# Optimization experiments

Hardware: AMD Instinct MI355X
Metric: run time of the kernel (lower is better)

Reference implementation:

```python
import jax, jax.numpy as jnp
import numpy as np

PI = 3.141592653589793
TAU = 0.5          # gumbel-softmax temperature
EPS = 1e-6
B, N, D = 128, 32, 256

def _linear(x, w, b=None):
    y = x @ w.T
    return y if b is None else y + b

def _wrap(a):
    return (a + PI) % (2 * PI) - PI

def setup_inputs() -> dict:
    key = jax.random.key(0)
    ks = jax.random.split(key, 16)
    s = 0.05
    return {
        "embedding": jax.random.normal(ks[0], (B, N, 11), jnp.float32),
        "gumbel_u": jax.random.uniform(ks[1], (B * N, N - 1, 2), jnp.float32),
        "emb1_w": jax.random.normal(ks[2], (128, 5), jnp.float32) * s,
        "emb1_b": jnp.zeros((128,), jnp.float32),
        "emb2_w": jax.random.normal(ks[3], (D, 128), jnp.float32) * s,
        "emb2_b": jnp.zeros((D,), jnp.float32),
        "hm1_w": jax.random.normal(ks[4], (D, D + 7), jnp.float32) * s,
        "hm1_b": jnp.zeros((D,), jnp.float32),
        "hm2_w": jax.random.normal(ks[5], (D, D), jnp.float32) * s,
        "hm2_b": jnp.zeros((D,), jnp.float32),
        "he_w": jax.random.normal(ks[6], (2, D), jnp.float32) * s,
        "he_b": jnp.zeros((2,), jnp.float32),
        "q_w": jax.random.normal(ks[7], (D, D), jnp.float32) * s,
        "k_w": jax.random.normal(ks[8], (D, 10), jnp.float32) * s,
        "v_w": jax.random.normal(ks[9], (D, 10), jnp.float32) * s,
        "v_b": jnp.zeros((D,), jnp.float32),
        "dec_w": jax.random.normal(ks[10], (2 * D, 2 * D), jnp.float32) * s,
        "dec_b": jnp.zeros((2 * D,), jnp.float32),
    }

def reference(embedding, gumbel_u, emb1_w, emb1_b, emb2_w, emb2_b,
              hm1_w, hm1_b, hm2_w, hm2_b, he_w, he_b,
              q_w, k_w, v_w, v_b, dec_w, dec_b):
    b, n, _ = embedding.shape
    d = q_w.shape[0]
    # static off-diagonal index lists (i,j), j != i, row-major like mask indexing
    rows, cols = np.nonzero(~np.eye(n, dtype=bool))

    embed = embedding[:, :, 4:9].reshape(b * n, 5)
    position = embedding[:, :, :2]
    heading = embedding[:, :, 2:4]
    action = embedding[:, :, 7:9]
    goal = embedding[:, :, -2:]

    # agent embedding MLP (leaky_relu slope 0.01, torch default)
    h = jax.nn.leaky_relu(_linear(embed, emb1_w, emb1_b))
    agent_embed = jax.nn.leaky_relu(_linear(h, emb2_w, emb2_b)).reshape(b, n, d)

    # pairwise geometry  [b,i,j,...]
    rel_vec = position[:, None, :, :] - position[:, :, None, :]   # pos_j - pos_i
    dx, dy = rel_vec[..., 0], rel_vec[..., 1]
    rel_dist = jnp.linalg.norm(rel_vec, axis=-1, keepdims=True) / 12.0
    heading_angle_i = jnp.arctan2(heading[..., 1], heading[..., 0])[:, :, None]  # [b,n,1]
    angle = _wrap(jnp.arctan2(dy, dx) - heading_angle_i)
    hj_cos = jnp.broadcast_to(heading[:, None, :, 0], (b, n, n))
    hj_sin = jnp.broadcast_to(heading[:, None, :, 1], (b, n, n))
    action_j = jnp.broadcast_to(action[:, None, :, :], (b, n, n, 2))
    edge_features = jnp.concatenate([
        rel_dist, jnp.cos(angle)[..., None], jnp.sin(angle)[..., None],
        hj_cos[..., None], hj_sin[..., None], action_j], axis=-1)  # [b,n,n,7]

    # hard attention branch (off-diagonal pairs only)
    h_i_flat = jnp.broadcast_to(agent_embed[:, :, None, :], (b, n, n - 1, d)).reshape(b * n, n - 1, d)
    edge_flat = edge_features[:, rows, cols].reshape(b * n, n - 1, 7)
    hard_input = jnp.concatenate([h_i_flat, edge_flat], axis=-1)
    h_hard = _linear(jax.nn.relu(_linear(hard_input, hm1_w, hm1_b)), hm2_w, hm2_b)
    hard_logits = _linear(h_hard, he_w, he_b)                      # [b*n, n-1, 2]
    g = -jnp.log(-jnp.log(gumbel_u + 1e-10) + 1e-10)
    hard_soft = jax.nn.softmax((hard_logits + g) / TAU, axis=-1)
    hard_weights = hard_soft[..., 1].reshape(b, n, n - 1)

    unnorm = jnp.linalg.norm(rel_vec, axis=-1, keepdims=True)      # [b,n,n,1]
    unnorm_rel_dist = unnorm[:, rows, cols].reshape(b * n, n - 1, 1)

    # goal polar features
    goal_rel_vec = goal[:, None, :, :] - position[:, :, None, :]   # [b,n,n,2]
    goal_rel_dist = jnp.linalg.norm(goal_rel_vec, axis=-1, keepdims=True)
    goal_rel_angle = _wrap(jnp.arctan2(goal_rel_vec[..., 1], goal_rel_vec[..., 0]) - heading_angle_i)
    goal_polar = jnp.concatenate([goal_rel_dist, jnp.cos(goal_rel_angle)[..., None],
                                  jnp.sin(goal_rel_angle)[..., None]], axis=-1)
    soft_edge = jnp.concatenate([edge_features, goal_polar], axis=-1)  # [b,n,n,10]

    # soft attention (vectorized over agents; off-diagonal gather)
    q = agent_embed @ q_w.T                                         # [b,n,d]
    k = soft_edge @ k_w.T                                           # [b,n,n,d]
    v = jax.nn.relu(_linear(soft_edge, v_w, v_b))                   # [b,n,n,d]
    k_off = k[:, rows, cols].reshape(b, n, n - 1, d)
    v_off = v[:, rows, cols].reshape(b, n, n - 1, d)
    score = jnp.einsum('bnd,bnjd->bnj', q, k_off) / jnp.sqrt(jnp.float32(d))
    soft_w = jax.nn.softmax(score, axis=-1)
    combined = soft_w * hard_weights                                # [b,n,n-1]
    x = jnp.einsum('bnjd,bnj->bnd', v_off, combined).reshape(b * n, d)

    final_input = jnp.concatenate([agent_embed.reshape(b * n, d), x], axis=-1)
    output = _linear(final_input, dec_w, dec_b)                     # [b*n, 2d]

    cwn = combined / (combined.sum(axis=-1, keepdims=True) + EPS)
    mean_entropy = (-(cwn * jnp.log(cwn + EPS)).sum(axis=-1)).mean()
    comb_w = combined.reshape(n, -1)  # matches torch.stack(dim=1).reshape(n, -1)

    return (output, hard_logits[..., 1], unnorm_rel_dist, mean_entropy, hard_weights, comb_w)
```

## Files before the change

kernel.cpp:

```cpp
#include <hip/hip_runtime.h>
#include <hip/hip_bf16.h>
#include <math.h>

typedef __hip_bfloat16 bf16;
typedef short bf16x8 __attribute__((ext_vector_type(8)));
typedef float f32x4 __attribute__((ext_vector_type(4)));
typedef unsigned short u16;

#define R_TOT 4096
#define NJ 31

#define OFF_AE   0
#define OFF_QK   1048576
#define OFF_S1   2097152
#define OFF_ENT  4542464
#define OFF_X    4546560
#define OFF_W    5595136
#define W_E1W   0
#define W_E1B   640
#define W_E2P   768
#define W_E2B   33536
#define W_H1B   101120
#define W_W1EP  167684
#define W_HE2P  171780
#define W_CB    173828
#define W_S1P   200452
#define W_VW    235780
#define W_VB    238340
#define W_DECWT 238596
#define W_DECB  500740
#define W_QKM   501252

#define OUT0 0
#define OUT1 2097152
#define OUT2 2224128
#define OUT3 2351104
#define OUT4 2351105
#define OUT5 2478081

__device__ __forceinline__ float b2f(bf16 x) { return __bfloat162float(x); }
__device__ __forceinline__ float ldin(const void* p, int i, int flag) {
    return flag ? b2f(((const bf16*)p)[i]) : ((const float*)p)[i];
}
__device__ __forceinline__ void stout(void* p, int i, float v, int flag) {
    if (flag) ((bf16*)p)[i] = __float2bfloat16(v);
    else      ((float*)p)[i] = v;
}
__device__ __forceinline__ u16 f2bbits(float v) {
    bf16 h = __float2bfloat16(v);
    return *(u16*)&h;
}
__device__ __forceinline__ int detect_flag(const void* emb) {
    float x = ((const float*)emb)[threadIdx.x & 63];
    int sane = (x == x) && (fabsf(x) < 1e20f);
    unsigned long long m = __ballot(sane);
    return (__popcll(m) == 64) ? 0 : 1;
}

__global__ __launch_bounds__(256) void k_prep(
        const void* emb,
        const void* e1w, const void* e1b, const void* e2w, const void* e2b,
        const void* h1w, const void* h1b, const void* h2w, const void* h2b,
        const void* hew, const void* heb, const void* qw,  const void* kw,
        const void* vw,  const void* vb,  const void* decw,const void* decb,
        float* W) {
    int flag = detect_flag(emb);
    int blk = blockIdx.x;
    int tid = threadIdx.x;
    if (blk < 2048) {
        int idx = blk * 256 + tid;
        if (idx < 262144) {
            int jj   = idx & 7;
            int lane = (idx >> 3) & 63;
            int tile = idx >> 9;
            int nt = tile & 31, kt = tile >> 5;
            int n = nt * 16 + (lane & 15);
            int k = kt * 32 + ((lane >> 4) << 3) + jj;
            ((u16*)(W + W_DECWT))[idx] = f2bbits(ldin(decw, n * 512 + k, flag));
        }
        int j = idx - 262144;
        if (j >= 0 && j < 98304) {
            int p;
            const void* src; int ldm, Wdst;
            if (j < 32768)      { p = j;          src = e2w; ldm = 128; Wdst = W_E2P; }
            else                { p = j - 32768;  src = h1w; ldm = 263; Wdst = W_S1P; }
            int jj   = p & 7;
            int lane = (p >> 3) & 63;
            int tile = p >> 9;
            int nt = tile & 15, kt = tile >> 4;
            int n = nt * 16 + (lane & 15);
            int k = kt * 32 + ((lane >> 4) << 3) + jj;
            ((u16*)(W + Wdst))[p] = f2bbits(ldin(src, n * ldm + k, flag));
        } else if (j >= 98304 && j < 102912) {
            int q2 = j - 98304;
            if      (q2 < 640)   W[W_E1W  + q2]           = ldin(e1w,  q2,          flag);
            else if (q2 < 768)   W[W_E1B  + (q2 - 640)]   = ldin(e1b,  q2 - 640,    flag);
            else if (q2 < 1024)  W[W_E2B  + (q2 - 768)]   = ldin(e2b,  q2 - 768,    flag);
            else if (q2 < 1280)  W[W_H1B  + (q2 - 1024)]  = ldin(h1b,  q2 - 1024,   flag);
            else if (q2 < 3840)  W[W_VW   + (q2 - 1280)]  = ldin(vw,   q2 - 1280,   flag);
            else if (q2 < 4096)  W[W_VB   + (q2 - 3840)]  = ldin(vb,   q2 - 3840,   flag);
            else                 W[W_DECB + (q2 - 4096)]  = ldin(decb, q2 - 4096,   flag);
        }
    } else if (blk < 2304) {
        int p = (blk - 2048) * 16 + (tid >> 4);
        int l = tid & 15;
        int jj = p & 7, lane = (p >> 3) & 63, kt = p >> 9;
        int k = kt * 32 + ((lane >> 4) << 3) + jj;
        int n = lane & 15;
        float v = 0.f;
        if (n < 10) {
#pragma unroll
            for (int dd = 0; dd < 16; dd++) {
                int d = l + 16 * dd;
                v += ldin(qw, d * 256 + k, flag) * ldin(kw, d * 10 + n, flag);
            }
        }
        v += __shfl_xor(v, 1, 64); v += __shfl_xor(v, 2, 64);
        v += __shfl_xor(v, 4, 64); v += __shfl_xor(v, 8, 64);
        if (l == 0) ((u16*)(W + W_QKM))[p] = f2bbits(v);
    } else if (blk < 2560) {
        int q = (blk - 2304) * 16 + (tid >> 4);
        int l = tid & 15;
        int jj = q & 7, lane = (q >> 3) & 63, kt = q >> 9;
        int n = lane & 15;
        int c = kt * 32 + ((lane >> 4) << 3) + jj;
        float v = 0.f;
        if (n < 2) {
#pragma unroll
            for (int dd = 0; dd < 16; dd++) {
                int d = l + 16 * dd;
                v += ldin(hew, n * 256 + d, flag) * ldin(h2w, d * 256 + c, flag);
            }
        }
        v += __shfl_xor(v, 1, 64); v += __shfl_xor(v, 2, 64);
        v += __shfl_xor(v, 4, 64); v += __shfl_xor(v, 8, 64);
        if (l == 0) ((u16*)(W + W_HE2P))[q] = f2bbits(v);
    } else if (blk < 2592) {
        int p = (blk - 2560) * 256 + tid;
        int jj = p & 7, lane = (p >> 3) & 63, nt = p >> 9;
        int n = nt * 16 + (lane & 15);
        int k = ((lane >> 4) << 3) + jj;
        float v = (k < 7) ? ldin(h1w, n * 263 + 256 + k, flag) : 0.f;
        ((u16*)(W + W_W1EP))[p] = f2bbits(v);
    } else {
        if (tid < 32) {
            int i = tid >> 4, l = tid & 15;
            float v = 0.f;
#pragma unroll
            for (int dd = 0; dd < 16; dd++) {
                int d = l + 16 * dd;
                v += ldin(hew, i * 256 + d, flag) * ldin(h2b, d, flag);
            }
            v += __shfl_xor(v, 1, 64); v += __shfl_xor(v, 2, 64);
            v += __shfl_xor(v, 4, 64); v += __shfl_xor(v, 8, 64);
            if (l == 0) W[W_CB + i] = v + ldin(heb, i, flag);
        }
    }
}

__global__ __launch_bounds__(256) void k_embed(const void* emb, const float* W,
                                               u16* aeb, float* qkws, float* s1ws) {
    int flag = detect_flag(emb);
    int r0 = blockIdx.x * 16;
    __shared__ float embL[16][12];
    __shared__ u16 hB[16][136];
    __shared__ u16 aeB[16][264];
    int tid = threadIdx.x;
    for (int idx = tid; idx < 16 * 11; idx += 256) {
        int s = idx / 11, t = idx % 11;
        embL[s][t] = ldin(emb, (r0 + s) * 11 + t, flag);
    }
    __syncthreads();
    for (int idx = tid; idx < 16 * 128; idx += 256) {
        int s = idx >> 7, jo = idx & 127;
        float v = W[W_E1B + jo];
#pragma unroll
        for (int t = 0; t < 5; t++) v += W[W_E1W + jo * 5 + t] * embL[s][4 + t];
        hB[s][jo] = f2bbits(v > 0.f ? v : 0.01f * v);
    }
    __syncthreads();
    int wv = tid >> 6, ln = tid & 63;
    int lr = ln & 15, quad = ln >> 4;
    {
        const bf16x8* Bp = (const bf16x8*)(W + W_E2P);
        f32x4 acc[4];
#pragma unroll
        for (int nt = 0; nt < 4; nt++) acc[nt] = (f32x4){0.f, 0.f, 0.f, 0.f};
#pragma unroll
        for (int kt = 0; kt < 4; kt++) {
            bf16x8 af = *(const bf16x8*)&hB[lr][kt * 32 + (quad << 3)];
#pragma unroll
            for (int nt = 0; nt < 4; nt++) {
                bf16x8 bfr = Bp[(kt * 16 + (wv * 4 + nt)) * 64 + ln];
                acc[nt] = __builtin_amdgcn_mfma_f32_16x16x32_bf16(af, bfr, acc[nt], 0, 0, 0);
            }
        }
#pragma unroll
        for (int nt = 0; nt < 4; nt++) {
            int d = wv * 64 + nt * 16 + lr;
            float bias = W[W_E2B + d];
#pragma unroll
            for (int reg = 0; reg < 4; reg++) {
                int m = quad * 4 + reg;
                float v = acc[nt][reg] + bias;
                v = v > 0.f ? v : 0.01f * v;
                u16 bits = f2bbits(v);
                aeB[m][d] = bits;
                aeb[(r0 + m) * 256 + d] = bits;
            }
        }
    }
    __syncthreads();
    {
        const bf16x8* Bs = (const bf16x8*)(W + W_S1P);
        f32x4 sac[4];
#pragma unroll
        for (int nt = 0; nt < 4; nt++) sac[nt] = (f32x4){0.f, 0.f, 0.f, 0.f};
#pragma unroll
        for (int kt = 0; kt < 8; kt++) {
            bf16x8 af = *(const bf16x8*)&aeB[lr][kt * 32 + (quad << 3)];
#pragma unroll
            for (int nt = 0; nt < 4; nt++) {
                bf16x8 bs = Bs[(kt * 16 + (wv * 4 + nt)) * 64 + ln];
                sac[nt] = __builtin_amdgcn_mfma_f32_16x16x32_bf16(af, bs, sac[nt], 0, 0, 0);
            }
        }
#pragma unroll
        for (int nt = 0; nt < 4; nt++) {
            int d = wv * 64 + nt * 16 + lr;
            float bias = W[W_H1B + d];
#pragma unroll
            for (int reg = 0; reg < 4; reg++) {
                int m = quad * 4 + reg;
                s1ws[(r0 + m) * 256 + d] = sac[nt][reg] + bias;
            }
        }
        if (wv == 0) {
            const bf16x8* Bm = (const bf16x8*)(W + W_QKM);
            f32x4 qk = (f32x4){0.f, 0.f, 0.f, 0.f};
#pragma unroll
            for (int kt = 0; kt < 8; kt++) {
                bf16x8 af = *(const bf16x8*)&aeB[lr][kt * 32 + (quad << 3)];
                qk = __builtin_amdgcn_mfma_f32_16x16x32_bf16(af, Bm[kt * 64 + ln], qk, 0, 0, 0);
            }
            if (lr < 10) {
#pragma unroll
                for (int reg = 0; reg < 4; reg++) {
                    int m = quad * 4 + reg;
                    qkws[(r0 + m) * 10 + lr] = qk[reg];
                }
            }
        }
    }
}

__global__ __launch_bounds__(256) void k_fused(const void* emb, const void* gum,
                                               const float* s1ws, const float* qkws, const float* W,
                                               u16* xb, float* entws, void* out) {
    int flag = detect_flag(emb);
    int r = blockIdx.x;
    int b = r >> 5, i = r & 31;
    __shared__ float embB[32][12];
    __shared__ float seL[32][10];
    __shared__ u16 eA[32][32];
    __shared__ u16 a1[32][264];
    __shared__ float pj[4][32][2];
    __shared__ float cL[32];
    __shared__ float qkL[10];
    int tid = threadIdx.x;
    for (int idx = tid; idx < 32 * 11; idx += 256) {
        int s = idx / 11, t = idx % 11;
        embB[s][t] = ldin(emb, (b * 32 + s) * 11 + t, flag);
    }
    for (int idx = tid; idx < 32 * 32; idx += 256) ((u16*)eA)[idx] = 0;
    if (tid >= 64 && tid < 74) qkL[tid - 64] = qkws[r * 10 + (tid - 64)];
    __syncthreads();
    if (tid < NJ) {
        int jp = tid;
        int j = jp + (jp >= i ? 1 : 0);
        float pix = embB[i][0], piy = embB[i][1], hix = embB[i][2], hiy = embB[i][3];
        float pjx = embB[j][0], pjy = embB[j][1], hjx = embB[j][2], hjy = embB[j][3];
        float ajx = embB[j][7], ajy = embB[j][8];
        float gjx = embB[j][9], gjy = embB[j][10];
        float dx = pjx - pix, dy = pjy - piy;
        float dist = sqrtf(dx * dx + dy * dy);
        float hai = atan2f(hiy, hix);
        float ang = atan2f(dy, dx) - hai;
        float gx = gjx - pix, gy = gjy - piy;
        float gdist = sqrtf(gx * gx + gy * gy);
        float gang = atan2f(gy, gx) - hai;
        float f[10];
        f[0] = dist * (1.f / 12.f);
        f[1] = cosf(ang); f[2] = sinf(ang);
        f[3] = hjx; f[4] = hjy; f[5] = ajx; f[6] = ajy;
        f[7] = gdist; f[8] = cosf(gang); f[9] = sinf(gang);
#pragma unroll
        for (int t = 0; t < 10; t++) seL[jp][t] = f[t];
#pragma unroll
        for (int t = 0; t < 7; t++) eA[jp][t] = f2bbits(f[t]);
        stout(out, OUT2 + r * NJ + jp, dist, flag);
    }
    __syncthreads();
    int wv = tid >> 6, ln = tid & 63;
    int lr = ln & 15, quad = ln >> 4;
    {
        const bf16x8* Bp = (const bf16x8*)(W + W_W1EP);
        bf16x8 af0 = *(const bf16x8*)&eA[lr][quad << 3];
        bf16x8 af1 = *(const bf16x8*)&eA[16 + lr][quad << 3];
#pragma unroll
        for (int nt = 0; nt < 4; nt++) {
            int gnt = wv * 4 + nt;
            int d = gnt * 16 + lr;
            float s1v = s1ws[r * 256 + d];
            f32x4 acc0 = (f32x4){s1v, s1v, s1v, s1v};
            f32x4 acc1 = acc0;
            bf16x8 bb = Bp[gnt * 64 + ln];
            acc0 = __builtin_amdgcn_mfma_f32_16x16x32_bf16(af0, bb, acc0, 0, 0, 0);
            acc1 = __builtin_amdgcn_mfma_f32_16x16x32_bf16(af1, bb, acc1, 0, 0, 0);
#pragma unroll
            for (int reg = 0; reg < 4; reg++) {
                a1[(quad << 2) + reg][d]      = f2bbits(fmaxf(acc0[reg], 0.f));
                a1[16 + (quad << 2) + reg][d] = f2bbits(fmaxf(acc1[reg], 0.f));
            }
        }
    }
    __syncthreads();
    {
        const bf16x8* Ep = (const bf16x8*)(W + W_HE2P);
        f32x4 l0 = (f32x4){0.f, 0.f, 0.f, 0.f};
        f32x4 l1 = (f32x4){0.f, 0.f, 0.f, 0.f};
#pragma unroll
        for (int kk = 0; kk < 2; kk++) {
            int kt = wv * 2 + kk;
            bf16x8 a0 = *(const bf16x8*)&a1[lr][kt * 32 + (quad << 3)];
            bf16x8 a1f = *(const bf16x8*)&a1[16 + lr][kt * 32 + (quad << 3)];
            bf16x8 bb = Ep[kt * 64 + ln];
            l0 = __builtin_amdgcn_mfma_f32_16x16x32_bf16(a0, bb, l0, 0, 0, 0);
            l1 = __builtin_amdgcn_mfma_f32_16x16x32_bf16(a1f, bb, l1, 0, 0, 0);
        }
        if (lr < 2) {
#pragma unroll
            for (int reg = 0; reg < 4; reg++) {
                pj[wv][(quad << 2) + reg][lr]      = l0[reg];
                pj[wv][16 + (quad << 2) + reg][lr] = l1[reg];
            }
        }
    }
    __syncthreads();
    if (wv == 0) {
        float hwv = 0.f;
        if (ln < NJ) {
            float p0 = pj[0][ln][0] + pj[1][ln][0] + pj[2][ln][0] + pj[3][ln][0];
            float p1 = pj[0][ln][1] + pj[1][ln][1] + pj[2][ln][1] + pj[3][ln][1];
            float l0 = p0 + W[W_CB + 0], l1 = p1 + W[W_CB + 1];
            float u0 = ldin(gum, (r * NJ + ln) * 2 + 0, flag);
            float u1 = ldin(gum, (r * NJ + ln) * 2 + 1, flag);
            float g0 = -logf(-logf(u0 + 1e-10f) + 1e-10f);
            float g1 = -logf(-logf(u1 + 1e-10f) + 1e-10f);
            float dl = ((l1 + g1) - (l0 + g0)) * 2.0f;
            hwv = 1.f / (1.f + expf(-dl));
            stout(out, OUT1 + r * NJ + ln, l1, flag);
            stout(out, OUT4 + r * NJ + ln, hwv, flag);
        }
        float sc = -1e30f;
        if (ln < NJ) {
            float p = 0.f;
#pragma unroll
            for (int t = 0; t < 10; t++) p += qkL[t] * seL[ln][t];
            sc = p * (1.f / 16.f);
        }
        float m = sc;
#pragma unroll
        for (int s = 32; s >= 1; s >>= 1) m = fmaxf(m, __shfl_xor(m, s, 64));
        float e = (ln < NJ) ? expf(sc - m) : 0.f;
        float sum = e;
#pragma unroll
        for (int s = 32; s >= 1; s >>= 1) sum += __shfl_xor(sum, s, 64);
        float sw = e / sum;
        float cmb = sw * hwv;
        if (ln < NJ) {
            cL[ln] = cmb;
            stout(out, OUT5 + r * NJ + ln, cmb, flag);
        }
        float csum = cmb;
#pragma unroll
        for (int s = 32; s >= 1; s >>= 1) csum += __shfl_xor(csum, s, 64);
        float cwn = cmb / (csum + 1e-6f);
        float et = (ln < NJ) ? -cwn * logf(cwn + 1e-6f) : 0.f;
#pragma unroll
        for (int s = 32; s >= 1; s >>= 1) et += __shfl_xor(et, s, 64);
        if (ln == 0) entws[r] = et;
    }
    __syncthreads();
    float vwr[10];
#pragma unroll
    for (int t = 0; t < 10; t++) vwr[t] = W[W_VW + tid * 10 + t];
    float vbv = W[W_VB + tid];
    float x = 0.f;
    for (int j = 0; j < NJ; j++) {
        float v = vbv;
#pragma unroll
        for (int t = 0; t < 10; t++) v += vwr[t] * seL[j][t];
        v = fmaxf(v, 0.f);
        x += v * cL[j];
    }
    xb[r * 256 + tid] = f2bbits(x);
}

__global__ __launch_bounds__(256) void k_dec(const void* emb, const u16* aeb, const u16* xb,
                                             const float* W, const float* entws, void* out) {
    int flag = detect_flag(emb);
    int r0 = (blockIdx.x >> 2) * 32;
    int nq = blockIdx.x & 3;
    __shared__ u16 finB[32][520];
    int tid = threadIdx.x;
    for (int idx = tid; idx < 32 * 512; idx += 256) {
        int s = idx >> 9, c = idx & 511;
        finB[s][c] = (c < 256) ? aeb[(r0 + s) * 256 + c] : xb[(r0 + s) * 256 + (c - 256)];
    }
    __syncthreads();
    int wv = tid >> 6, ln = tid & 63;
    int lr = ln & 15, quad = ln >> 4;
    const bf16x8* Bp = (const bf16x8*)(W + W_DECWT);
    f32x4 acc[2][2];
#pragma unroll
    for (int mt = 0; mt < 2; mt++)
#pragma unroll
        for (int nt = 0; nt < 2; nt++) acc[mt][nt] = (f32x4){0.f, 0.f, 0.f, 0.f};
#pragma unroll
    for (int kt = 0; kt < 16; kt++) {
        bf16x8 af[2];
#pragma unroll
        for (int mt = 0; mt < 2; mt++)
            af[mt] = *(const bf16x8*)&finB[mt * 16 + lr][kt * 32 + (quad << 3)];
#pragma unroll
        for (int nt = 0; nt < 2; nt++) {
            int gnt = nq * 8 + wv * 2 + nt;
            bf16x8 bfr = Bp[(kt * 32 + gnt) * 64 + ln];
#pragma unroll
            for (int mt = 0; mt < 2; mt++)
                acc[mt][nt] = __builtin_amdgcn_mfma_f32_16x16x32_bf16(af[mt], bfr, acc[mt][nt], 0, 0, 0);
        }
    }
#pragma unroll
    for (int nt = 0; nt < 2; nt++) {
        int d = (nq * 8 + wv * 2 + nt) * 16 + lr;
        float bias = W[W_DECB + d];
#pragma unroll
        for (int mt = 0; mt < 2; mt++)
#pragma unroll
            for (int reg = 0; reg < 4; reg++) {
                int m = mt * 16 + quad * 4 + reg;
                stout(out, OUT0 + (r0 + m) * 512 + d, acc[mt][nt][reg] + bias, flag);
            }
    }
    if (blockIdx.x == 0) {
        __shared__ float red[4];
        float s = 0.f;
        for (int i2 = tid; i2 < R_TOT; i2 += 256) s += entws[i2];
#pragma unroll
        for (int m = 32; m >= 1; m >>= 1) s += __shfl_xor(s, m, 64);
        if ((tid & 63) == 0) red[tid >> 6] = s;
        __syncthreads();
        if (tid == 0) {
            float t = red[0] + red[1] + red[2] + red[3];
            stout(out, OUT3, t / (float)R_TOT, flag);
        }
    }
}

extern "C" void kernel_launch(void* const* d_in, const int* in_sizes, int n_in,
                              void* d_out, int out_size, void* d_ws, size_t ws_size,
                              hipStream_t stream) {
    const void* emb  = d_in[0];
    const void* gum  = d_in[1];
    const void* e1w  = d_in[2];
    const void* e1b  = d_in[3];
    const void* e2w  = d_in[4];
    const void* e2b  = d_in[5];
    const void* h1w  = d_in[6];
    const void* h1b  = d_in[7];
    const void* h2w  = d_in[8];
    const void* h2b  = d_in[9];
    const void* hew  = d_in[10];
    const void* heb  = d_in[11];
    const void* qw   = d_in[12];
    const void* kw   = d_in[13];
    const void* vw   = d_in[14];
    const void* vb   = d_in[15];
    const void* decw = d_in[16];
    const void* decb = d_in[17];

    float* wsf = (float*)d_ws;
    u16*   aeb  = (u16*)(wsf + OFF_AE);
    float* qkws = wsf + OFF_QK;
    float* s1ws = wsf + OFF_S1;
    float* entw = wsf + OFF_ENT;
    u16*   xb   = (u16*)(wsf + OFF_X);
    float* W    = wsf + OFF_W;

    hipLaunchKernelGGL(k_prep, dim3(2593), dim3(256), 0, stream,
                       emb, e1w, e1b, e2w, e2b, h1w, h1b, h2w, h2b, hew, heb,
                       qw, kw, vw, vb, decw, decb, W);
    hipLaunchKernelGGL(k_embed, dim3(256), dim3(256), 0, stream, emb, W, aeb, qkws, s1ws);
    hipLaunchKernelGGL(k_fused, dim3(4096), dim3(256), 0, stream,
                       emb, gum, s1ws, qkws, W, xb, entw, d_out);
    hipLaunchKernelGGL(k_dec, dim3(512), dim3(256), 0, stream, emb, aeb, xb, W, entw, d_out);
}
```

Before: 161.1 us.

## Move weight packing not needed by embed into the embed kernel launch

Weight-prep work is split across two kernels. The first keeps only what k_embed depends on: the e2/h1 packing, the QK product and the small vectors. The decoder weight transpose, the he·h2 product, the W1E packing and the constant bias now run as extra blocks of k_embed, so they overlap with the embedding computation. This shrinks the serial prep kernel on the critical path, at the cost of a larger k_embed grid with mixed block roles.

```diff
diff --git a/kernel.cpp b/kernel.cpp
--- a/kernel.cpp
+++ b/kernel.cpp
@@ -60,16 +60,63 @@
 __global__ __launch_bounds__(256) void k_prep(
         const void* emb,
         const void* e1w, const void* e1b, const void* e2w, const void* e2b,
-        const void* h1w, const void* h1b, const void* h2w, const void* h2b,
-        const void* hew, const void* heb, const void* qw,  const void* kw,
-        const void* vw,  const void* vb,  const void* decw,const void* decb,
+        const void* h1w, const void* h1b, const void* qw,  const void* kw,
+        const void* vw,  const void* vb,  const void* decb,
         float* W) {
     int flag = detect_flag(emb);
     int blk = blockIdx.x;
     int tid = threadIdx.x;
-    if (blk < 2048) {
-        int idx = blk * 256 + tid;
-        if (idx < 262144) {
+    if (blk < 384) {
+        int p; const void* src; int ldm, Wdst;
+        if (blk < 128) { p = blk * 256 + tid;         src = e2w; ldm = 128; Wdst = W_E2P; }
+        else           { p = (blk - 128) * 256 + tid; src = h1w; ldm = 263; Wdst = W_S1P; }
+        int jj   = p & 7;
+        int lane = (p >> 3) & 63;
+        int tile = p >> 9;
+        int nt = tile & 15, kt = tile >> 4;
+        int n = nt * 16 + (lane & 15);
+        int k = kt * 32 + ((lane >> 4) << 3) + jj;
+        ((u16*)(W + Wdst))[p] = f2bbits(ldin(src, n * ldm + k, flag));
+    } else if (blk < 640) {
+        int p = (blk - 384) * 16 + (tid >> 4);
+        int l = tid & 15;
+        int jj = p & 7, lane = (p >> 3) & 63, kt = p >> 9;
+        int k = kt * 32 + ((lane >> 4) << 3) + jj;
+        int n = lane & 15;
+        float v = 0.f;
+        if (n < 10) {
+#pragma unroll
+            for (int dd = 0; dd < 16; dd++) {
+                int d = l + 16 * dd;
+                v += ldin(qw, d * 256 + k, flag) * ldin(kw, d * 10 + n, flag);
+            }
+        }
+        v += __shfl_xor(v, 1, 64); v += __shfl_xor(v, 2, 64);
+        v += __shfl_xor(v, 4, 64); v += __shfl_xor(v, 8, 64);
+        if (l == 0) ((u16*)(W + W_QKM))[p] = f2bbits(v);
+    } else {
+        int q2 = (blk - 640) * 256 + tid;
+        if      (q2 < 640)   W[W_E1W  + q2]           = ldin(e1w,  q2,          flag);
+        else if (q2 < 768)   W[W_E1B  + (q2 - 640)]   = ldin(e1b,  q2 - 640,    flag);
+        else if (q2 < 1024)  W[W_E2B  + (q2 - 768)]   = ldin(e2b,  q2 - 768,    flag);
+        else if (q2 < 1280)  W[W_H1B  + (q2 - 1024)]  = ldin(h1b,  q2 - 1024,   flag);
+        else if (q2 < 3840)  W[W_VW   + (q2 - 1280)]  = ldin(vw,   q2 - 1280,   flag);
+        else if (q2 < 4096)  W[W_VB   + (q2 - 3840)]  = ldin(vb,   q2 - 3840,   flag);
+        else if (q2 < 4608)  W[W_DECB + (q2 - 4096)]  = ldin(decb, q2 - 4096,   flag);
+    }
+}
+
+__global__ __launch_bounds__(256) void k_embed(const void* emb, const float* W_,
+                                               const void* h1w, const void* h2w, const void* h2b,
+                                               const void* hew, const void* heb, const void* decw,
+                                               u16* aeb, float* qkws, float* s1ws) {
+    int flag = detect_flag(emb);
+    float* W = (float*)W_;
+    int blk = blockIdx.x;
+    int tid = threadIdx.x;
+    if (blk >= 256) {
+        if (blk < 1280) {
+            int idx = (blk - 256) * 256 + tid;
             int jj   = idx & 7;
             int lane = (idx >> 3) & 63;
             int tile = idx >> 9;
@@ -77,95 +124,50 @@
             int n = nt * 16 + (lane & 15);
             int k = kt * 32 + ((lane >> 4) << 3) + jj;
             ((u16*)(W + W_DECWT))[idx] = f2bbits(ldin(decw, n * 512 + k, flag));
-        }
-        int j = idx - 262144;
-        if (j >= 0 && j < 98304) {
-            int p;
-            const void* src; int ldm, Wdst;
-            if (j < 32768)      { p = j;          src = e2w; ldm = 128; Wdst = W_E2P; }
-            else                { p = j - 32768;  src = h1w; ldm = 263; Wdst = W_S1P; }
-            int jj   = p & 7;
-            int lane = (p >> 3) & 63;
-            int tile = p >> 9;
-            int nt = tile & 15, kt = tile >> 4;
+        } else if (blk < 1312) {
+            int p = (blk - 1280) * 256 + tid;
+            int jj = p & 7, lane = (p >> 3) & 63, nt = p >> 9;
             int n = nt * 16 + (lane & 15);
-            int k = kt * 32 + ((lane >> 4) << 3) + jj;
-            ((u16*)(W + Wdst))[p] = f2bbits(ldin(src, n * ldm + k, flag));
-        } else if (j >= 98304 && j < 102912) {
-            int q2 = j - 98304;
-            if      (q2 < 640)   W[W_E1W  + q2]           = ldin(e1w,  q2,          flag);
-            else if (q2 < 768)   W[W_E1B  + (q2 - 640)]   = ldin(e1b,  q2 - 640,    flag);
-            else if (q2 < 1024)  W[W_E2B  + (q2 - 768)]   = ldin(e2b,  q2 - 768,    flag);
-            else if (q2 < 1280)  W[W_H1B  + (q2 - 1024)]  = ldin(h1b,  q2 - 1024,   flag);
-            else if (q2 < 3840)  W[W_VW   + (q2 - 1280)]  = ldin(vw,   q2 - 1280,   flag);
-            else if (q2 < 4096)  W[W_VB   + (q2 - 3840)]  = ldin(vb,   q2 - 3840,   flag);
-            else                 W[W_DECB + (q2 - 4096)]  = ldin(decb, q2 - 4096,   flag);
-        }
-    } else if (blk < 2304) {
-        int p = (blk - 2048) * 16 + (tid >> 4);
-        int l = tid & 15;
-        int jj = p & 7, lane = (p >> 3) & 63, kt = p >> 9;
-        int k = kt * 32 + ((lane >> 4) << 3) + jj;
-        int n = lane & 15;
-        float v = 0.f;
-        if (n < 10) {
-#pragma unroll
-            for (int dd = 0; dd < 16; dd++) {
-                int d = l + 16 * dd;
-                v += ldin(qw, d * 256 + k, flag) * ldin(kw, d * 10 + n, flag);
-            }
-        }
-        v += __shfl_xor(v, 1, 64); v += __shfl_xor(v, 2, 64);
-        v += __shfl_xor(v, 4, 64); v += __shfl_xor(v, 8, 64);
-        if (l == 0) ((u16*)(W + W_QKM))[p] = f2bbits(v);
-    } else if (blk < 2560) {
-        int q = (blk - 2304) * 16 + (tid >> 4);
-        int l = tid & 15;
-        int jj = q & 7, lane = (q >> 3) & 63, kt = q >> 9;
-        int n = lane & 15;
-        int c = kt * 32 + ((lane >> 4) << 3) + jj;
-        float v = 0.f;
-        if (n < 2) {
-#pragma unroll
-            for (int dd = 0; dd < 16; dd++) {
-                int d = l + 16 * dd;
-                v += ldin(hew, n * 256 + d, flag) * ldin(h2w, d * 256 + c, flag);
-            }
-        }
-        v += __shfl_xor(v, 1, 64); v += __shfl_xor(v, 2, 64);
-        v += __shfl_xor(v, 4, 64); v += __shfl_xor(v, 8, 64);
-        if (l == 0) ((u16*)(W + W_HE2P))[q] = f2bbits(v);
-    } else if (blk < 2592) {
-        int p = (blk - 2560) * 256 + tid;
-        int jj = p & 7, lane = (p >> 3) & 63, nt = p >> 9;
-        int n = nt * 16 + (lane & 15);
-        int k = ((lane >> 4) << 3) + jj;
-        float v = (k < 7) ? ldin(h1w, n * 263 + 256 + k, flag) : 0.f;
-        ((u16*)(W + W_W1EP))[p] = f2bbits(v);
-    } else {
-        if (tid < 32) {
-            int i = tid >> 4, l = tid & 15;
+            int k = ((lane >> 4) << 3) + jj;
+            float v = (k < 7) ? ldin(h1w, n * 263 + 256 + k, flag) : 0.f;
+            ((u16*)(W + W_W1EP))[p] = f2bbits(v);
+        } else if (blk < 1568) {
+            int q = (blk - 1312) * 16 + (tid >> 4);
+            int l = tid & 15;
+            int jj = q & 7, lane = (q >> 3) & 63, kt = q >> 9;
+            int n = lane & 15;
+            int c = kt * 32 + ((lane >> 4) << 3) + jj;
             float v = 0.f;
-#pragma unroll
-            for (int dd = 0; dd < 16; dd++) {
-                int d = l + 16 * dd;
-                v += ldin(hew, i * 256 + d, flag) * ldin(h2b, d, flag);
+            if (n < 2) {
+#pragma unroll
+                for (int dd = 0; dd < 16; dd++) {
+                    int d = l + 16 * dd;
+                    v += ldin(hew, n * 256 + d, flag) * ldin(h2w, d * 256 + c, flag);
+                }
             }
             v += __shfl_xor(v, 1, 64); v += __shfl_xor(v, 2, 64);
             v += __shfl_xor(v, 4, 64); v += __shfl_xor(v, 8, 64);
-            if (l == 0) W[W_CB + i] = v + ldin(heb, i, flag);
-        }
-    }
-}
-
-__global__ __launch_bounds__(256) void k_embed(const void* emb, const float* W,
-                                               u16* aeb, float* qkws, float* s1ws) {
-    int flag = detect_flag(emb);
-    int r0 = blockIdx.x * 16;
+            if (l == 0) ((u16*)(W + W_HE2P))[q] = f2bbits(v);
+        } else {
+            if (tid < 32) {
+                int i = tid >> 4, l = tid & 15;
+                float v = 0.f;
+#pragma unroll
+                for (int dd = 0; dd < 16; dd++) {
+                    int d = l + 16 * dd;
+                    v += ldin(hew, i * 256 + d, flag) * ldin(h2b, d, flag);
+                }
+                v += __shfl_xor(v, 1, 64); v += __shfl_xor(v, 2, 64);
+                v += __shfl_xor(v, 4, 64); v += __shfl_xor(v, 8, 64);
+                if (l == 0) W[W_CB + i] = v + ldin(heb, i, flag);
+            }
+        }
+        return;
+    }
+    int r0 = blk * 16;
     __shared__ float embL[16][12];
     __shared__ u16 hB[16][136];
     __shared__ u16 aeB[16][264];
-    int tid = threadIdx.x;
     for (int idx = tid; idx < 16 * 11; idx += 256) {
         int s = idx / 11, t = idx % 11;
         embL[s][t] = ldin(emb, (r0 + s) * 11 + t, flag);
@@ -499,10 +501,10 @@
     u16*   xb   = (u16*)(wsf + OFF_X);
     float* W    = wsf + OFF_W;
 
-    hipLaunchKernelGGL(k_prep, dim3(2593), dim3(256), 0, stream,
-                       emb, e1w, e1b, e2w, e2b, h1w, h1b, h2w, h2b, hew, heb,
-                       qw, kw, vw, vb, decw, decb, W);
-    hipLaunchKernelGGL(k_embed, dim3(256), dim3(256), 0, stream, emb, W, aeb, qkws, s1ws);
+    hipLaunchKernelGGL(k_prep, dim3(659), dim3(256), 0, stream,
+                       emb, e1w, e1b, e2w, e2b, h1w, h1b, qw, kw, vw, vb, decb, W);
+    hipLaunchKernelGGL(k_embed, dim3(1569), dim3(256), 0, stream,
+                       emb, W, h1w, h2w, h2b, hew, heb, decw, aeb, qkws, s1ws);
     hipLaunchKernelGGL(k_fused, dim3(4096), dim3(256), 0, stream,
                        emb, gum, s1ws, qkws, W, xb, entw, d_out);
     hipLaunchKernelGGL(k_dec, dim3(512), dim3(256), 0, stream, emb, aeb, xb, W, entw, d_out);
```

After: 155.2 us. 3.7% less time.
